# Optimization experiments

Measured on AMD Instinct MI355X. Metric: run time of the kernel, lower is better.

Reference implementation:

```python
import jax, jax.numpy as jnp
import numpy as np

DIM = 2048
K_DIM = 2048
HQ = 16          # query heads
HKV = 4          # kv heads
HD = DIM // HQ   # head dim = 128
KV_DIM = HD * HKV
MAX_LEN = 4096
THETA = 10000.0
ROPE_FACTOR = 8.0
CAUSAL = True
SCALE = HD ** -0.5


def rope_cos_sin(n):
    # mirrors generate_sin_cos_pos_emb (rope_factor > 1 branch)
    idx = jnp.arange(0, HD, 2, dtype=jnp.float32) / HD
    seq_len_eff = max(n, MAX_LEN)  # static python ints
    base_adjustment = (ROPE_FACTOR * seq_len_eff / MAX_LEN - (ROPE_FACTOR - 1.0)) ** (HD / (HD - 2))
    inv_freq = 1.0 / (THETA * base_adjustment) ** idx
    pos = jnp.arange(n, dtype=jnp.float32)
    if not CAUSAL:
        pos = pos - (n - 1) // 2
    freqs = pos[:, None] * inv_freq[None, :]          # [n, HD/2]
    emb = jnp.concatenate([freqs, freqs], axis=-1)    # [n, HD]
    return jnp.cos(emb), jnp.sin(emb)


def rotate_half(x):
    x1, x2 = jnp.split(x, 2, axis=-1)
    return jnp.concatenate([-x2, x1], axis=-1)


def setup_inputs() -> dict:
    key = jax.random.key(0)
    ks = jax.random.split(key, 11)
    B, N = 2, 2048
    s = 0.02
    return {
        "query": jax.random.normal(ks[0], (B, N, DIM), jnp.float32),
        "key": jax.random.normal(ks[1], (B, N, K_DIM), jnp.float32),
        "value": jax.random.normal(ks[2], (B, N, K_DIM), jnp.float32),
        "Wq": jax.random.normal(ks[3], (DIM, DIM), jnp.float32) * s,
        "bq": jnp.zeros((DIM,), jnp.float32),
        "Wk": jax.random.normal(ks[4], (KV_DIM, K_DIM), jnp.float32) * s,
        "bk": jnp.zeros((KV_DIM,), jnp.float32),
        "Wv": jax.random.normal(ks[5], (KV_DIM, K_DIM), jnp.float32) * s,
        "bv": jnp.zeros((KV_DIM,), jnp.float32),
        "Wo": jax.random.normal(ks[6], (DIM, DIM), jnp.float32) * s,
        "bo": jnp.zeros((DIM,), jnp.float32),
    }


def reference(query, key, value, Wq, bq, Wk, bk, Wv, bv, Wo, bo):
    b, n, _ = query.shape
    q = query @ Wq.T + bq                       # [b, n, DIM]
    k = key @ Wk.T + bk                         # [b, n, KV_DIM]
    v = value @ Wv.T + bv                       # [b, n, KV_DIM]
    q = q.reshape(b, n, HQ, HD).transpose(0, 2, 1, 3)    # [b, HQ, n, d]
    k = k.reshape(b, n, HKV, HD).transpose(0, 2, 1, 3)   # [b, HKV, n, d]
    v = v.reshape(b, n, HKV, HD).transpose(0, 2, 1, 3)
    cos, sin = rope_cos_sin(n)                  # [n, HD] each, broadcast over b,h
    q = q * cos + rotate_half(q) * sin
    k = k * cos + rotate_half(k) * sin
    g = HQ // HKV
    qg = q.reshape(b, HKV, g, n, HD)            # group query heads per kv head
    scores = jnp.einsum('bhgnd,bhsd->bhgns', qg * SCALE, k)  # [b, HKV, g, n, s]
    if CAUSAL:
        causal = jnp.tril(jnp.ones((n, n), dtype=bool))
        scores = jnp.where(causal[None, None, None], scores, jnp.finfo(scores.dtype).min)
    attn = jax.nn.softmax(scores, axis=-1)
    out = jnp.einsum('bhgns,bhsd->bhgnd', attn, v)           # [b, HKV, g, n, d]
    out = out.reshape(b, HQ, n, HD).transpose(0, 2, 1, 3).reshape(b, n, DIM)
    return out @ Wo.T + bo
```

## Files before the change

kernel.cpp:

```cpp
#include <hip/hip_runtime.h>
#include <cstdint>


typedef __bf16 bf16_t;
typedef __attribute__((ext_vector_type(8))) __bf16 bf16x8;
typedef __attribute__((ext_vector_type(4))) float f32x4;

#define B_    2
#define N_    2048
#define DIM_  2048
#define HQ_   16
#define HKV_  4
#define HD_   128
#define KVD_  512
#define SCALE_ 0.08838834764831845f

static __device__ __forceinline__ void ld_g2l(void* lds, const void* g) {
  __builtin_amdgcn_global_load_lds((__attribute__((address_space(1))) void*)g,
                                   (__attribute__((address_space(3))) void*)lds,
                                   16, 0, 0);
}

static __device__ __forceinline__ f32x4 vmax4(f32x4 a, f32x4 b) {
  f32x4 r;
  r[0] = fmaxf(a[0], b[0]); r[1] = fmaxf(a[1], b[1]);
  r[2] = fmaxf(a[2], b[2]); r[3] = fmaxf(a[3], b[3]);
  return r;
}

__global__ void k_sincos(float* __restrict__ cosT, float* __restrict__ sinT) {
  int idx = blockIdx.x * 256 + threadIdx.x;
  int i = idx & 63;
  int n = idx >> 6;
  float inv = expf(-(float)i * (9.210340371976184f / 64.0f));
  float ang = (float)n * inv;
  cosT[idx] = cosf(ang);
  sinT[idx] = sinf(ang);
}

__global__ void k_cvt3(const float* __restrict__ s0, bf16_t* __restrict__ d0, int n0,
                       const float* __restrict__ s1, bf16_t* __restrict__ d1, int n1,
                       const float* __restrict__ s2, bf16_t* __restrict__ d2, int n2)
{
  int i = (blockIdx.x * 256 + threadIdx.x) * 4;
  const float* s; bf16_t* d; int off;
  if (i < n0)                { s = s0; d = d0; off = i; }
  else if (i < n0 + n1)      { s = s1; d = d1; off = i - n0; }
  else if (i < n0 + n1 + n2) { s = s2; d = d2; off = i - n0 - n1; }
  else return;
  f32x4 v = *(const f32x4*)(s + off);
  union { bf16_t h[4]; uint2 u; } pk;
  pk.h[0] = (bf16_t)v[0]; pk.h[1] = (bf16_t)v[1];
  pk.h[2] = (bf16_t)v[2]; pk.h[3] = (bf16_t)v[3];
  *(uint2*)(d + off) = pk.u;
}

template <int AMODE, bool CF32>
static __device__ __forceinline__ void gemm_body(
    const void* __restrict__ Av, const bf16_t* __restrict__ W,
    const float* __restrict__ bias, void* __restrict__ Cv,
    int N, int K, int bm, int bn, bf16_t* As, bf16_t* Bs)
{
  const int tid  = threadIdx.x;
  const int lane = tid & 63;
  const int wave = tid >> 6;
  const int l15  = lane & 15;
  const int lg   = lane >> 4;
  const int wr = (wave >> 1) * 32, wc = (wave & 1) * 64;

  f32x4 acc[2][4] = {};

  uint8_t* AsB = (uint8_t*)As;
  uint8_t* BsB = (uint8_t*)Bs;
  const uint8_t* Wbase = (const uint8_t*)W + (size_t)(bn * 128) * K * 2;
  const uint8_t* AbaseB = (const uint8_t*)Av + (size_t)(bm * 64) * K * 2;

  for (int k0 = 0; k0 < K; k0 += 64) {
    for (int r = 0; r < 4; ++r) {
      int o = r * 4096 + wave * 1024 + lane * 16;
      int row = o >> 7;
      int colB = (o & 127) ^ ((row & 7) << 4);
      ld_g2l(BsB + r * 4096 + wave * 1024,
             Wbase + (size_t)row * (K * 2) + (size_t)k0 * 2 + colB);
    }
    if (AMODE == 1) {
      for (int r = 0; r < 2; ++r) {
        int o = r * 4096 + wave * 1024 + lane * 16;
        int row = o >> 7;
        int colB = (o & 127) ^ ((row & 7) << 4);
        ld_g2l(AsB + r * 4096 + wave * 1024,
               AbaseB + (size_t)row * (K * 2) + (size_t)k0 * 2 + colB);
      }
    } else {
      for (int i = 0; i < 2; ++i) {
        int c = i * 256 + tid;
        int row = c >> 3;
        int k8  = (c & 7) * 8;
        const float* ap = (const float*)Av + (size_t)(bm * 64 + row) * K + k0 + k8;
        f32x4 alo = *(const f32x4*)ap;
        f32x4 ahi = *(const f32x4*)(ap + 4);
        bf16x8 va;
        va[0] = (bf16_t)alo[0]; va[1] = (bf16_t)alo[1];
        va[2] = (bf16_t)alo[2]; va[3] = (bf16_t)alo[3];
        va[4] = (bf16_t)ahi[0]; va[5] = (bf16_t)ahi[1];
        va[6] = (bf16_t)ahi[2]; va[7] = (bf16_t)ahi[3];
        int sw = (k8 * 2) ^ ((row & 7) << 4);
        *(bf16x8*)(AsB + row * 128 + sw) = va;
      }
    }
    __syncthreads();
    for (int kk = 0; kk < 2; ++kk) {
      const int koff = kk * 64 + (lg << 4);
      bf16x8 fa[2], fb[4];
      for (int fi = 0; fi < 2; ++fi) {
        int row = wr + fi * 16 + l15;
        fa[fi] = *(const bf16x8*)(AsB + row * 128 + (koff ^ ((row & 7) << 4)));
      }
      for (int fj = 0; fj < 4; ++fj) {
        int row = wc + fj * 16 + l15;
        fb[fj] = *(const bf16x8*)(BsB + row * 128 + (koff ^ ((row & 7) << 4)));
      }
      for (int fi = 0; fi < 2; ++fi)
        for (int fj = 0; fj < 4; ++fj)
          acc[fi][fj] = __builtin_amdgcn_mfma_f32_16x16x32_bf16(
              fa[fi], fb[fj], acc[fi][fj], 0, 0, 0);
    }
    __syncthreads();
  }

  const int r0 = lg * 4;
  for (int fi = 0; fi < 2; ++fi) {
    for (int rr = 0; rr < 4; ++rr) {
      int grow = bm * 64 + wr + fi * 16 + r0 + rr;
      size_t rowoff = (size_t)grow * N;
      for (int fj = 0; fj < 4; ++fj) {
        int gcol = bn * 128 + wc + fj * 16 + l15;
        float v = acc[fi][fj][rr] + bias[gcol];
        if (CF32) ((float*)Cv)[rowoff + gcol] = v;
        else      ((bf16_t*)Cv)[rowoff + gcol] = (bf16_t)v;
      }
    }
  }
}

__global__ __launch_bounds__(256, 4) void k_gemm_qkv(
    const float* __restrict__ q, const bf16_t* __restrict__ Wqb,
    const float* __restrict__ bq, bf16_t* __restrict__ Qp,
    const float* __restrict__ k, const bf16_t* __restrict__ Wkb,
    const float* __restrict__ bk, bf16_t* __restrict__ Kp,
    const float* __restrict__ v, const bf16_t* __restrict__ Wvb,
    const float* __restrict__ bv, bf16_t* __restrict__ Vp)
{
  __shared__ bf16_t As[64 * 64];
  __shared__ bf16_t Bs[128 * 64];
  const int z = blockIdx.z;
  if (z != 0 && blockIdx.y >= 4) return;
  const float* A; const bf16_t* W; const float* bias; bf16_t* C; int Nn;
  if (z == 0)      { A = q; W = Wqb; bias = bq; C = Qp; Nn = 2048; }
  else if (z == 1) { A = k; W = Wkb; bias = bk; C = Kp; Nn = 512; }
  else             { A = v; W = Wvb; bias = bv; C = Vp; Nn = 512; }
  gemm_body<0, false>(A, W, bias, C, Nn, 2048, blockIdx.x, blockIdx.y, As, Bs);
}

__global__ __launch_bounds__(256, 4) void k_gemm_o(
    const bf16_t* __restrict__ Ain, const bf16_t* __restrict__ Wob,
    const float* __restrict__ bo, float* __restrict__ out)
{
  __shared__ bf16_t As[64 * 64];
  __shared__ bf16_t Bs[128 * 64];
  gemm_body<1, true>(Ain, Wob, bo, out, 2048, 2048, blockIdx.x, blockIdx.y, As, Bs);
}

__global__ void k_rope(bf16_t* __restrict__ X, const float* __restrict__ cosT,
                       const float* __restrict__ sinT, int lgnh, float outScale)
{
  int idx = blockIdx.x * 256 + threadIdx.x;
  int j = idx & 7;
  int h = (idx >> 3) & ((1 << lgnh) - 1);
  int row = idx >> (3 + lgnh);
  int n = row & (N_ - 1);
  int d0 = j * 8;
  const float* cp = cosT + (n << 6) + d0;
  const float* sp = sinT + (n << 6) + d0;
  f32x4 c0 = *(const f32x4*)cp,  c1 = *(const f32x4*)(cp + 4);
  f32x4 s0 = *(const f32x4*)sp,  s1 = *(const f32x4*)(sp + 4);
  bf16_t* xb = X + (size_t)row * (size_t)(128 << lgnh) + (h << 7) + d0;
  bf16x8 x1 = *(const bf16x8*)xb;
  bf16x8 x2 = *(const bf16x8*)(xb + 64);
  bf16x8 o1, o2;
#pragma unroll
  for (int e = 0; e < 8; ++e) {
    float c = e < 4 ? c0[e] : c1[e - 4];
    float s = e < 4 ? s0[e] : s1[e - 4];
    float a = (float)x1[e], bvl = (float)x2[e];
    o1[e] = (bf16_t)((a * c - bvl * s) * outScale);
    o2[e] = (bf16_t)((bvl * c + a * s) * outScale);
  }
  *(bf16x8*)xb = o1;
  *(bf16x8*)(xb + 64) = o2;
}

__global__ void k_transpose_v(const bf16_t* __restrict__ Vp, bf16_t* __restrict__ Vt)
{
  __shared__ bf16_t tile[64][72];
  const int tid = threadIdx.x;
  const int r0 = blockIdx.x * 64;
  const int d0 = blockIdx.y * 64;
  for (int r = 0; r < 2; ++r) {
    int n = r * 32 + (tid >> 3);
    int dc = (tid & 7) * 8;
    *(uint4*)&tile[n][dc] = *(const uint4*)(Vp + (size_t)(r0 + n) * KVD_ + d0 + dc);
  }
  __syncthreads();
  const int b = r0 >> 11;
  const int nseq = r0 & (N_ - 1);
  for (int r = 0; r < 2; ++r) {
    int dd = r * 32 + (tid >> 3);
    int nc = (tid & 7) * 8;
    int dglob = d0 + dd;
    int hkv = dglob >> 7, dloc = dglob & 127;
    union { bf16_t h[8]; uint4 v; } pk;
    for (int j = 0; j < 8; ++j) pk.h[j] = tile[nc + j][dd];
    size_t drow = (size_t)(b * HKV_ + hkv) * 128 + dloc;
    *(uint4*)(Vt + drow * N_ + nseq + nc) = pk.v;
  }
}

__global__ __launch_bounds__(256, 2) void k_attn(
    const bf16_t* __restrict__ Qp, const bf16_t* __restrict__ Kp,
    const bf16_t* __restrict__ Vt, bf16_t* __restrict__ AO)
{
  __shared__ bf16_t Ks[2][64 * 128];
  __shared__ bf16_t Vs[2][128 * 64];
  __shared__ bf16_t Ps[4][16 * 72];
  const int tid = threadIdx.x, lane = tid & 63, wave = tid >> 6;
  const int l15 = lane & 15, lg = lane >> 4;
  const int bx = 15 - (int)blockIdx.x;
  const int qtile = bx * 4 + wave;
  const int bh = blockIdx.y;
  const int b = bh >> 4, hq = bh & 15, hkv = hq >> 2;

  bf16x8 qf[2][4];
  for (int rf = 0; rf < 2; ++rf) {
    size_t qrow = (size_t)b * N_ + qtile * 32 + rf * 16 + l15;
    const uint8_t* qb = (const uint8_t*)Qp + (qrow * DIM_ + (size_t)hq * HD_) * 2 + lg * 16;
    for (int ks = 0; ks < 4; ++ks)
      qf[rf][ks] = *(const bf16x8*)(qb + ks * 64);
  }

  float m[2] = {-1e30f, -1e30f};
  float ln[2] = {0.f, 0.f};
  f32x4 o[2][8] = {};

  const uint8_t* KpB = (const uint8_t*)Kp + ((size_t)b * N_ * KVD_ + (size_t)hkv * HD_) * 2;
  const uint8_t* VtB = (const uint8_t*)Vt + (size_t)(b * HKV_ + hkv) * HD_ * (size_t)N_ * 2;
  uint8_t* PwB = (uint8_t*)Ps[wave];

  const int Tw   = qtile / 2 + 1;
  const int Tmax = 2 * bx + 2;

  auto stage = [&](int buf, int t) {
    uint8_t* KsB = (uint8_t*)Ks[buf];
    uint8_t* VsB = (uint8_t*)Vs[buf];
#pragma unroll
    for (int r = 0; r < 4; ++r) {
      int o16 = r * 4096 + wave * 1024 + lane * 16;
      int row = o16 >> 8;
      int colB = (o16 & 255) ^ ((row & 7) << 4);
      ld_g2l(KsB + r * 4096 + wave * 1024,
             KpB + (size_t)(t * 64 + row) * (KVD_ * 2) + colB);
    }
#pragma unroll
    for (int r = 0; r < 4; ++r) {
      int o16 = r * 4096 + wave * 1024 + lane * 16;
      int dd = o16 >> 7;
      int colB = (o16 & 127) ^ ((dd & 7) << 4);
      ld_g2l(VsB + r * 4096 + wave * 1024,
             VtB + (size_t)dd * (N_ * 2) + t * 128 + colB);
    }
  };

  stage(0, 0);
  __syncthreads();
  int cur = 0;

  for (int t = 0; t < Tmax; ++t) {
    if (t + 1 < Tmax) stage(cur ^ 1, t + 1);

    if (t < Tw) {
      const uint8_t* KsB = (const uint8_t*)Ks[cur];
      const uint8_t* VsB = (const uint8_t*)Vs[cur];

      f32x4 s4[2][4] = {};
      __builtin_amdgcn_s_setprio(1);
#pragma unroll
      for (int ks = 0; ks < 4; ++ks) {
        int koff = ks * 64 + lg * 16;
#pragma unroll
        for (int kb = 0; kb < 4; ++kb) {
          int row = kb * 16 + l15;
          bf16x8 kf = *(const bf16x8*)(KsB + row * 256 + (koff ^ ((row & 7) << 4)));
          s4[0][kb] = __builtin_amdgcn_mfma_f32_16x16x32_bf16(kf, qf[0][ks], s4[0][kb], 0, 0, 0);
          s4[1][kb] = __builtin_amdgcn_mfma_f32_16x16x32_bf16(kf, qf[1][ks], s4[1][kb], 0, 0, 0);
        }
      }
      __builtin_amdgcn_s_setprio(0);

      if (t == Tw - 1) {
#pragma unroll
        for (int rf = 0; rf < 2; ++rf) {
          int q = qtile * 32 + rf * 16 + l15;
#pragma unroll
          for (int kb = 0; kb < 4; ++kb) {
            int key = t * 64 + kb * 16 + lg * 4;
#pragma unroll
            for (int rr = 0; rr < 4; ++rr)
              if (key + rr > q) s4[rf][kb][rr] = -1e30f;
          }
        }
      }

      bf16x8 pf[2][2];
#pragma unroll
      for (int rf = 0; rf < 2; ++rf) {
        f32x4 mx = vmax4(vmax4(s4[rf][0], s4[rf][1]), vmax4(s4[rf][2], s4[rf][3]));
        float rm = fmaxf(fmaxf(mx[0], mx[1]), fmaxf(mx[2], mx[3]));
        rm = fmaxf(rm, __shfl_xor(rm, 16));
        rm = fmaxf(rm, __shfl_xor(rm, 32));
        float mn = fmaxf(m[rf], rm);
        float sc = __expf(m[rf] - mn);

        f32x4 p[4];
        f32x4 psum = {0.f, 0.f, 0.f, 0.f};
#pragma unroll
        for (int kb = 0; kb < 4; ++kb) {
#pragma unroll
          for (int rr = 0; rr < 4; ++rr)
            p[kb][rr] = __expf(s4[rf][kb][rr] - mn);
          psum += p[kb];
        }
        float rs = (psum[0] + psum[1]) + (psum[2] + psum[3]);
        rs += __shfl_xor(rs, 16);
        rs += __shfl_xor(rs, 32);
        ln[rf] = ln[rf] * sc + rs;
        m[rf] = mn;

#pragma unroll
        for (int db = 0; db < 8; ++db) o[rf][db] *= sc;

#pragma unroll
        for (int kb = 0; kb < 4; ++kb) {
          union { bf16_t h[4]; uint2 u; } pk;
          pk.h[0] = (bf16_t)p[kb][0]; pk.h[1] = (bf16_t)p[kb][1];
          pk.h[2] = (bf16_t)p[kb][2]; pk.h[3] = (bf16_t)p[kb][3];
          *(uint2*)(PwB + l15 * 144 + kb * 32 + lg * 8) = pk.u;
        }
        pf[rf][0] = *(const bf16x8*)(PwB + l15 * 144 + lg * 16);
        pf[rf][1] = *(const bf16x8*)(PwB + l15 * 144 + 64 + lg * 16);
      }

      __builtin_amdgcn_s_setprio(1);
#pragma unroll
      for (int ks2 = 0; ks2 < 2; ++ks2) {
        int koff = ks2 * 64 + lg * 16;
#pragma unroll
        for (int db = 0; db < 8; ++db) {
          int dd = db * 16 + l15;
          bf16x8 vf = *(const bf16x8*)(VsB + dd * 128 + (koff ^ ((dd & 7) << 4)));
          o[0][db] = __builtin_amdgcn_mfma_f32_16x16x32_bf16(vf, pf[0][ks2], o[0][db], 0, 0, 0);
          o[1][db] = __builtin_amdgcn_mfma_f32_16x16x32_bf16(vf, pf[1][ks2], o[1][db], 0, 0, 0);
        }
      }
      __builtin_amdgcn_s_setprio(0);
    }

    __syncthreads();
    cur ^= 1;
  }

#pragma unroll
  for (int rf = 0; rf < 2; ++rf) {
    float iv = 1.f / ln[rf];
    size_t qrow = (size_t)b * N_ + qtile * 32 + rf * 16 + l15;
    uint8_t* ob = (uint8_t*)(AO + qrow * DIM_ + (size_t)hq * HD_);
#pragma unroll
    for (int db = 0; db < 8; ++db) {
      union { bf16_t h[4]; uint2 u; } pk;
      pk.h[0] = (bf16_t)(o[rf][db][0] * iv);
      pk.h[1] = (bf16_t)(o[rf][db][1] * iv);
      pk.h[2] = (bf16_t)(o[rf][db][2] * iv);
      pk.h[3] = (bf16_t)(o[rf][db][3] * iv);
      *(uint2*)(ob + (db * 16 + lg * 4) * 2) = pk.u;
    }
  }
}

extern "C" void kernel_launch(void* const* d_in, const int* in_sizes, int n_in,
                              void* d_out, int out_size, void* d_ws, size_t ws_size,
                              hipStream_t stream)
{
  if (ws_size < (46u << 20)) return;

  const float* query = (const float*)d_in[0];
  const float* key   = (const float*)d_in[1];
  const float* value = (const float*)d_in[2];
  const float* Wq = (const float*)d_in[3];
  const float* bq = (const float*)d_in[4];
  const float* Wk = (const float*)d_in[5];
  const float* bk = (const float*)d_in[6];
  const float* Wv = (const float*)d_in[7];
  const float* bv = (const float*)d_in[8];
  const float* Wo = (const float*)d_in[9];
  const float* bo = (const float*)d_in[10];
  float* out = (float*)d_out;

  uint8_t* ws = (uint8_t*)d_ws;
  float*  cosT = (float*)(ws);
  float*  sinT = (float*)(ws + (512u << 10));
  bf16_t* Qp   = (bf16_t*)(ws + (1u  << 20));
  bf16_t* Kp   = (bf16_t*)(ws + (17u << 20));
  bf16_t* Vp   = (bf16_t*)(ws + (21u << 20));
  bf16_t* Vt   = (bf16_t*)(ws + (25u << 20));
  bf16_t* Wqb  = (bf16_t*)(ws + (29u << 20));
  bf16_t* Wkb  = (bf16_t*)(ws + (37u << 20));
  bf16_t* Wvb  = (bf16_t*)(ws + (39u << 20));
  bf16_t* Wob  = (bf16_t*)(ws + (17u << 20));

  k_sincos<<<512, 256, 0, stream>>>(cosT, sinT);

  k_cvt3<<<6144, 256, 0, stream>>>(Wq, Wqb, 4194304,
                                   Wk, Wkb, 1048576,
                                   Wv, Wvb, 1048576);

  k_gemm_qkv<<<dim3(64, 16, 3), 256, 0, stream>>>(
      query, Wqb, bq, Qp, key, Wkb, bk, Kp, value, Wvb, bv, Vp);

  k_rope<<<2048, 256, 0, stream>>>(Qp, cosT, sinT, 4, SCALE_);
  k_rope<<<512,  256, 0, stream>>>(Kp, cosT, sinT, 2, 1.0f);

  k_transpose_v<<<dim3(64, 8), 256, 0, stream>>>(Vp, Vt);

  k_attn<<<dim3(16, 32), 256, 0, stream>>>(Qp, Kp, Vt, Qp);

  k_cvt3<<<4096, 256, 0, stream>>>(Wo, Wob, 4194304,
                                   nullptr, nullptr, 0,
                                   nullptr, nullptr, 0);

  k_gemm_o<<<dim3(64, 16), 256, 0, stream>>>(Qp, Wob, bo, out);
}
```

Before: 245.2 us.

## Double K-tile depth and prefetch fp32 A into registers in GEMM

The GEMM main loop now consumes a 128-wide K slice per iteration instead of 64, which halves the number of barrier pairs per tile. The fp32 activation path loads the next A tile into registers before the MFMA loop, so the global read overlaps compute, and converts it to bf16 on the next iteration. s_setprio is raised around the MFMA block. In exchange, LDS use doubles to 48 KB per block and register pressure rises, and launch bounds are cut from 4 to 3 blocks per CU, which lowers occupancy.

```diff
diff --git a/kernel.cpp b/kernel.cpp
--- a/kernel.cpp
+++ b/kernel.cpp
@@ -74,65 +74,100 @@
   uint8_t* BsB = (uint8_t*)Bs;
   const uint8_t* Wbase = (const uint8_t*)W + (size_t)(bn * 128) * K * 2;
   const uint8_t* AbaseB = (const uint8_t*)Av + (size_t)(bm * 64) * K * 2;
-
-  for (int k0 = 0; k0 < K; k0 += 64) {
+  const float*   Af = (const float*)Av;
+
+  f32x4 areg[8];
+
+  auto loadA = [&](int k0) {
+#pragma unroll
+    for (int i = 0; i < 4; ++i) {
+      int c = i * 256 + tid;
+      int row = c >> 4;
+      int k8  = (c & 15) * 8;
+      const float* ap = Af + (size_t)(bm * 64 + row) * K + k0 + k8;
+      areg[i * 2]     = *(const f32x4*)ap;
+      areg[i * 2 + 1] = *(const f32x4*)(ap + 4);
+    }
+  };
+  auto writeA = [&]() {
+#pragma unroll
+    for (int i = 0; i < 4; ++i) {
+      int c = i * 256 + tid;
+      int row = c >> 4;
+      int k8  = (c & 15) * 8;
+      bf16x8 va;
+      f32x4 lo = areg[i * 2], hi = areg[i * 2 + 1];
+      va[0] = (bf16_t)lo[0]; va[1] = (bf16_t)lo[1];
+      va[2] = (bf16_t)lo[2]; va[3] = (bf16_t)lo[3];
+      va[4] = (bf16_t)hi[0]; va[5] = (bf16_t)hi[1];
+      va[6] = (bf16_t)hi[2]; va[7] = (bf16_t)hi[3];
+      int sw = (k8 * 2) ^ ((row & 7) << 4);
+      *(bf16x8*)(AsB + row * 256 + sw) = va;
+    }
+  };
+  auto stageW = [&](int k0) {
+#pragma unroll
+    for (int r = 0; r < 8; ++r) {
+      int o = r * 4096 + wave * 1024 + lane * 16;
+      int row = o >> 8;
+      int colB = (o & 255) ^ ((row & 7) << 4);
+      ld_g2l(BsB + r * 4096 + wave * 1024,
+             Wbase + (size_t)row * (K * 2) + (size_t)k0 * 2 + colB);
+    }
+  };
+  auto stageA_g2l = [&](int k0) {
+#pragma unroll
     for (int r = 0; r < 4; ++r) {
       int o = r * 4096 + wave * 1024 + lane * 16;
-      int row = o >> 7;
-      int colB = (o & 127) ^ ((row & 7) << 4);
-      ld_g2l(BsB + r * 4096 + wave * 1024,
-             Wbase + (size_t)row * (K * 2) + (size_t)k0 * 2 + colB);
-    }
-    if (AMODE == 1) {
-      for (int r = 0; r < 2; ++r) {
-        int o = r * 4096 + wave * 1024 + lane * 16;
-        int row = o >> 7;
-        int colB = (o & 127) ^ ((row & 7) << 4);
-        ld_g2l(AsB + r * 4096 + wave * 1024,
-               AbaseB + (size_t)row * (K * 2) + (size_t)k0 * 2 + colB);
-      }
-    } else {
-      for (int i = 0; i < 2; ++i) {
-        int c = i * 256 + tid;
-        int row = c >> 3;
-        int k8  = (c & 7) * 8;
-        const float* ap = (const float*)Av + (size_t)(bm * 64 + row) * K + k0 + k8;
-        f32x4 alo = *(const f32x4*)ap;
-        f32x4 ahi = *(const f32x4*)(ap + 4);
-        bf16x8 va;
-        va[0] = (bf16_t)alo[0]; va[1] = (bf16_t)alo[1];
-        va[2] = (bf16_t)alo[2]; va[3] = (bf16_t)alo[3];
-        va[4] = (bf16_t)ahi[0]; va[5] = (bf16_t)ahi[1];
-        va[6] = (bf16_t)ahi[2]; va[7] = (bf16_t)ahi[3];
-        int sw = (k8 * 2) ^ ((row & 7) << 4);
-        *(bf16x8*)(AsB + row * 128 + sw) = va;
-      }
-    }
+      int row = o >> 8;
+      int colB = (o & 255) ^ ((row & 7) << 4);
+      ld_g2l(AsB + r * 4096 + wave * 1024,
+             AbaseB + (size_t)row * (K * 2) + (size_t)k0 * 2 + colB);
+    }
+  };
+
+  if (AMODE == 0) loadA(0);
+
+  for (int k0 = 0; k0 < K; k0 += 128) {
+    stageW(k0);
+    if (AMODE == 0) writeA();
+    else            stageA_g2l(k0);
     __syncthreads();
-    for (int kk = 0; kk < 2; ++kk) {
+    if (AMODE == 0 && k0 + 128 < K) loadA(k0 + 128);
+    __builtin_amdgcn_s_setprio(1);
+#pragma unroll
+    for (int kk = 0; kk < 4; ++kk) {
       const int koff = kk * 64 + (lg << 4);
       bf16x8 fa[2], fb[4];
+#pragma unroll
       for (int fi = 0; fi < 2; ++fi) {
         int row = wr + fi * 16 + l15;
-        fa[fi] = *(const bf16x8*)(AsB + row * 128 + (koff ^ ((row & 7) << 4)));
-      }
+        fa[fi] = *(const bf16x8*)(AsB + row * 256 + (koff ^ ((row & 7) << 4)));
+      }
+#pragma unroll
       for (int fj = 0; fj < 4; ++fj) {
         int row = wc + fj * 16 + l15;
-        fb[fj] = *(const bf16x8*)(BsB + row * 128 + (koff ^ ((row & 7) << 4)));
-      }
+        fb[fj] = *(const bf16x8*)(BsB + row * 256 + (koff ^ ((row & 7) << 4)));
+      }
+#pragma unroll
       for (int fi = 0; fi < 2; ++fi)
+#pragma unroll
         for (int fj = 0; fj < 4; ++fj)
           acc[fi][fj] = __builtin_amdgcn_mfma_f32_16x16x32_bf16(
               fa[fi], fb[fj], acc[fi][fj], 0, 0, 0);
     }
+    __builtin_amdgcn_s_setprio(0);
     __syncthreads();
   }
 
   const int r0 = lg * 4;
+#pragma unroll
   for (int fi = 0; fi < 2; ++fi) {
+#pragma unroll
     for (int rr = 0; rr < 4; ++rr) {
       int grow = bm * 64 + wr + fi * 16 + r0 + rr;
       size_t rowoff = (size_t)grow * N;
+#pragma unroll
       for (int fj = 0; fj < 4; ++fj) {
         int gcol = bn * 128 + wc + fj * 16 + l15;
         float v = acc[fi][fj][rr] + bias[gcol];
@@ -143,7 +178,7 @@
   }
 }
 
-__global__ __launch_bounds__(256, 4) void k_gemm_qkv(
+__global__ __launch_bounds__(256, 3) void k_gemm_qkv(
     const float* __restrict__ q, const bf16_t* __restrict__ Wqb,
     const float* __restrict__ bq, bf16_t* __restrict__ Qp,
     const float* __restrict__ k, const bf16_t* __restrict__ Wkb,
@@ -151,8 +186,8 @@
     const float* __restrict__ v, const bf16_t* __restrict__ Wvb,
     const float* __restrict__ bv, bf16_t* __restrict__ Vp)
 {
-  __shared__ bf16_t As[64 * 64];
-  __shared__ bf16_t Bs[128 * 64];
+  __shared__ bf16_t As[64 * 128];
+  __shared__ bf16_t Bs[128 * 128];
   const int z = blockIdx.z;
   if (z != 0 && blockIdx.y >= 4) return;
   const float* A; const bf16_t* W; const float* bias; bf16_t* C; int Nn;
@@ -162,12 +197,12 @@
   gemm_body<0, false>(A, W, bias, C, Nn, 2048, blockIdx.x, blockIdx.y, As, Bs);
 }
 
-__global__ __launch_bounds__(256, 4) void k_gemm_o(
+__global__ __launch_bounds__(256, 3) void k_gemm_o(
     const bf16_t* __restrict__ Ain, const bf16_t* __restrict__ Wob,
     const float* __restrict__ bo, float* __restrict__ out)
 {
-  __shared__ bf16_t As[64 * 64];
-  __shared__ bf16_t Bs[128 * 64];
+  __shared__ bf16_t As[64 * 128];
+  __shared__ bf16_t Bs[128 * 128];
   gemm_body<1, true>(Ain, Wob, bo, out, 2048, 2048, blockIdx.x, blockIdx.y, As, Bs);
 }
 
```

Result: slower. 257.8 us (+5.2%).
